# Performance work log

Hardware: AMD Instinct MI355X
Metric: run time of the kernel (lower is better)

The kernel has to match this reference:

```python
import jax, jax.numpy as jnp
import numpy as np

EMB = 768

def _mlp2(x, Wa, Wb):
    # relu(LL2(relu(LL1(x)))), bias-free linears stored as [out, in]
    return jax.nn.relu(jax.nn.relu(x @ Wa.T) @ Wb.T)

def setup_inputs() -> dict:
    key = jax.random.key(0)
    ks = jax.random.split(key, 6)
    n, m = 16, 4096  # maxlen = 64 paragraphs -> 64*64 pair slots
    X_data = jax.random.normal(ks[0], (n, 1 + m, 3 * EMB), dtype=jnp.float32)
    # first token carries num_clusters metadata (unused by the differentiable path)
    W1 = jax.random.normal(ks[1], (256, EMB), dtype=jnp.float32) * 0.02
    W2 = jax.random.normal(ks[2], (128, 256), dtype=jnp.float32) * 0.02
    W3 = jax.random.normal(ks[3], (256, EMB), dtype=jnp.float32) * 0.02
    W4 = jax.random.normal(ks[4], (128, 256), dtype=jnp.float32) * 0.02
    W5 = jax.random.normal(ks[5], (1, 128), dtype=jnp.float32) * 0.02
    return {"X_data": X_data, "W1": W1, "W2": W2, "W3": W3, "W4": W4, "W5": W5}

def reference(X_data, W1, W2, W3, W4, W5):
    # CATSCluster differentiable path: QueryScaler on X_data[:, 1:, :]
    X = X_data[:, 1:, :]                      # [n, m, 3*EMB]
    Xq = X[..., :EMB]
    Xp1 = X[..., EMB:2 * EMB]
    Xp2 = X[..., 2 * EMB:]
    Xp1z = _mlp2(Xp1, W1, W2)                 # [n, m, 128]
    Xp2z = _mlp2(Xp2, W1, W2)
    Xqz = _mlp2(Xq, W3, W4)
    Xpqz = Xqz * jnp.abs(Xp1z - Xp2z)         # [n, m, 128]
    dist = jnp.tanh(jax.nn.relu(Xpqz @ W5.T))[..., 0]  # [n, m]
    n, m = dist.shape
    p = int(np.sqrt(m))                       # maxlen
    # batch_pairscore_matrix fed to the host-side clustering step
    return dist.reshape(n, p, p)
```

## Files before the change

### kernel.cpp

```cpp
#include <hip/hip_runtime.h>
#include <hip/hip_bf16.h>


typedef short short8 __attribute__((ext_vector_type(8)));
typedef float f32x4 __attribute__((ext_vector_type(4)));

#define W1H_OFF 0u
#define W1L_OFF 196608u
#define W3H_OFF 393216u
#define W3L_OFF 589824u
#define W2H_OFF 786432u
#define W2L_OFF 819200u
#define W4H_OFF 851968u
#define W4L_OFF 884736u

__device__ __forceinline__ unsigned short bf16_rne(float f) {
  unsigned int u = __float_as_uint(f);
  u += 0x7FFFu + ((u >> 16) & 1u);
  return (unsigned short)(u >> 16);
}

__device__ __forceinline__ void split_bf16(float f, unsigned short& h, unsigned short& l) {
  h = bf16_rne(f);
  float fh = __uint_as_float(((unsigned int)h) << 16);
  l = bf16_rne(f - fh);
}

__global__ __launch_bounds__(256) void prep_weights(
    const float* __restrict__ W1, const float* __restrict__ W2,
    const float* __restrict__ W3, const float* __restrict__ W4,
    unsigned short* __restrict__ ws)
{
  int i = blockIdx.x * 256 + threadIdx.x;
  if (i < 196608) {
    unsigned short h, l;
    split_bf16(W1[i], h, l); ws[W1H_OFF + i] = h; ws[W1L_OFF + i] = l;
    split_bf16(W3[i], h, l); ws[W3H_OFF + i] = h; ws[W3L_OFF + i] = l;
    if (i < 32768) {
      split_bf16(W2[i], h, l); ws[W2H_OFF + i] = h; ws[W2L_OFF + i] = l;
      split_bf16(W4[i], h, l); ws[W4H_OFF + i] = h; ws[W4L_OFF + i] = l;
    }
  }
}

#define STRIDE_A 40
#define STRIDE_H 264

__global__ __launch_bounds__(256) void catsc_main(
    const float* __restrict__ X, const unsigned short* __restrict__ ws,
    const float* __restrict__ W5, float* __restrict__ out)
{
  __shared__ short lsA[2][2][64 * STRIDE_A];
  __shared__ short lsH[64 * STRIDE_H];
  __shared__ float lsPart[4][64];

  const int tid  = threadIdx.x;
  const int wave = tid >> 6;
  const int lane = tid & 63;
  const int l15  = lane & 15;
  const int q    = lane >> 4;
  const int blk  = blockIdx.x;

  const float* Xb = X + (size_t)((blk >> 6) * 4097 + 1 + ((blk & 63) << 6)) * 2304;

  const int srow = tid >> 3;
  const int f4   = (tid & 7) << 2;

  f32x4 z[3][4][2];

#pragma unroll
  for (int s = 0; s < 3; ++s) {
    const unsigned short* B1h = ws + (s == 0 ? W3H_OFF : W1H_OFF);
    const unsigned short* B1l = ws + (s == 0 ? W3L_OFF : W1L_OFF);
    const unsigned short* B2h = ws + (s == 0 ? W4H_OFF : W2H_OFF);
    const unsigned short* B2l = ws + (s == 0 ? W4L_OFF : W2L_OFF);
    const int so = s * 768;

    f32x4 acc[4][4];
#pragma unroll
    for (int m = 0; m < 4; ++m)
#pragma unroll
      for (int n = 0; n < 4; ++n)
        acc[m][n] = f32x4{0.f, 0.f, 0.f, 0.f};

#pragma unroll
    for (int it = 0; it < 2; ++it) {
      int rr = srow + 32 * it;
      float4 v = *(const float4*)(Xb + (size_t)rr * 2304 + so + f4);
      unsigned short h0,h1,h2,h3,l0,l1,l2,l3;
      split_bf16(v.x,h0,l0); split_bf16(v.y,h1,l1);
      split_bf16(v.z,h2,l2); split_bf16(v.w,h3,l3);
      uint2 ph, pl;
      ph.x = (unsigned)h0 | ((unsigned)h1 << 16); ph.y = (unsigned)h2 | ((unsigned)h3 << 16);
      pl.x = (unsigned)l0 | ((unsigned)l1 << 16); pl.y = (unsigned)l2 | ((unsigned)l3 << 16);
      *(uint2*)&lsA[0][0][rr * STRIDE_A + f4] = ph;
      *(uint2*)&lsA[0][1][rr * STRIDE_A + f4] = pl;
    }
    __syncthreads();

    for (int c = 0; c < 24; ++c) {
      const int b = c & 1;
      if (c + 1 < 24) {
        const int nb = b ^ 1;
#pragma unroll
        for (int it = 0; it < 2; ++it) {
          int rr = srow + 32 * it;
          float4 v = *(const float4*)(Xb + (size_t)rr * 2304 + so + (c + 1) * 32 + f4);
          unsigned short h0,h1,h2,h3,l0,l1,l2,l3;
          split_bf16(v.x,h0,l0); split_bf16(v.y,h1,l1);
          split_bf16(v.z,h2,l2); split_bf16(v.w,h3,l3);
          uint2 ph, pl;
          ph.x = (unsigned)h0 | ((unsigned)h1 << 16); ph.y = (unsigned)h2 | ((unsigned)h3 << 16);
          pl.x = (unsigned)l0 | ((unsigned)l1 << 16); pl.y = (unsigned)l2 | ((unsigned)l3 << 16);
          *(uint2*)&lsA[nb][0][rr * STRIDE_A + f4] = ph;
          *(uint2*)&lsA[nb][1][rr * STRIDE_A + f4] = pl;
        }
      }
      short8 Bh[4], Bl[4];
#pragma unroll
      for (int n = 0; n < 4; ++n) {
        size_t off = (size_t)((wave * 4 + n) * 16 + l15) * 768 + c * 32 + q * 8;
        Bh[n] = *(const short8*)(B1h + off);
        Bl[n] = *(const short8*)(B1l + off);
      }
      short8 Ah[4], Al[4];
#pragma unroll
      for (int m = 0; m < 4; ++m) {
        int a = (m * 16 + l15) * STRIDE_A + q * 8;
        Ah[m] = *(const short8*)&lsA[b][0][a];
        Al[m] = *(const short8*)&lsA[b][1][a];
      }
#pragma unroll
      for (int m = 0; m < 4; ++m)
#pragma unroll
        for (int n = 0; n < 4; ++n)
          acc[m][n] = __builtin_amdgcn_mfma_f32_16x16x32_bf16(Ah[m], Bh[n], acc[m][n], 0, 0, 0);
#pragma unroll
      for (int m = 0; m < 4; ++m)
#pragma unroll
        for (int n = 0; n < 4; ++n)
          acc[m][n] = __builtin_amdgcn_mfma_f32_16x16x32_bf16(Ah[m], Bl[n], acc[m][n], 0, 0, 0);
#pragma unroll
      for (int m = 0; m < 4; ++m)
#pragma unroll
        for (int n = 0; n < 4; ++n)
          acc[m][n] = __builtin_amdgcn_mfma_f32_16x16x32_bf16(Al[m], Bh[n], acc[m][n], 0, 0, 0);
      __syncthreads();
    }

#pragma unroll
    for (int m = 0; m < 4; ++m)
#pragma unroll
      for (int n = 0; n < 4; ++n) {
        int col = (wave * 4 + n) * 16 + l15;
#pragma unroll
        for (int i = 0; i < 4; ++i) {
          int row = m * 16 + q * 4 + i;
          lsH[row * STRIDE_H + col] = bf16_rne(fmaxf(acc[m][n][i], 0.f));
        }
      }
    __syncthreads();

    f32x4 acc2[4][2];
#pragma unroll
    for (int m = 0; m < 4; ++m)
#pragma unroll
      for (int n = 0; n < 2; ++n)
        acc2[m][n] = f32x4{0.f, 0.f, 0.f, 0.f};

    for (int c2 = 0; c2 < 8; ++c2) {
      short8 Ch[2], Cl[2];
#pragma unroll
      for (int n2 = 0; n2 < 2; ++n2) {
        size_t off = (size_t)((wave * 2 + n2) * 16 + l15) * 256 + c2 * 32 + q * 8;
        Ch[n2] = *(const short8*)(B2h + off);
        Cl[n2] = *(const short8*)(B2l + off);
      }
      short8 Ha[4];
#pragma unroll
      for (int m = 0; m < 4; ++m)
        Ha[m] = *(const short8*)&lsH[(m * 16 + l15) * STRIDE_H + c2 * 32 + q * 8];
#pragma unroll
      for (int m = 0; m < 4; ++m)
#pragma unroll
        for (int n2 = 0; n2 < 2; ++n2)
          acc2[m][n2] = __builtin_amdgcn_mfma_f32_16x16x32_bf16(Ha[m], Ch[n2], acc2[m][n2], 0, 0, 0);
#pragma unroll
      for (int m = 0; m < 4; ++m)
#pragma unroll
        for (int n2 = 0; n2 < 2; ++n2)
          acc2[m][n2] = __builtin_amdgcn_mfma_f32_16x16x32_bf16(Ha[m], Cl[n2], acc2[m][n2], 0, 0, 0);
    }
#pragma unroll
    for (int m = 0; m < 4; ++m)
#pragma unroll
      for (int n2 = 0; n2 < 2; ++n2)
#pragma unroll
        for (int i = 0; i < 4; ++i)
          z[s][m][n2][i] = fmaxf(acc2[m][n2][i], 0.f);
  }

  const float w5c0 = W5[(wave * 2 + 0) * 16 + l15];
  const float w5c1 = W5[(wave * 2 + 1) * 16 + l15];
#pragma unroll
  for (int m = 0; m < 4; ++m) {
#pragma unroll
    for (int i = 0; i < 4; ++i) {
      float v = z[0][m][0][i] * fabsf(z[1][m][0][i] - z[2][m][0][i]) * w5c0
              + z[0][m][1][i] * fabsf(z[1][m][1][i] - z[2][m][1][i]) * w5c1;
      v += __shfl_xor(v, 1);
      v += __shfl_xor(v, 2);
      v += __shfl_xor(v, 4);
      v += __shfl_xor(v, 8);
      if (l15 == 0) lsPart[wave][m * 16 + q * 4 + i] = v;
    }
  }
  __syncthreads();
  if (tid < 64) {
    float sum = lsPart[0][tid] + lsPart[1][tid] + lsPart[2][tid] + lsPart[3][tid];
    out[(size_t)blk * 64 + tid] = tanhf(fmaxf(sum, 0.f));
  }
}

extern "C" void kernel_launch(void* const* d_in, const int* in_sizes, int n_in,
                              void* d_out, int out_size, void* d_ws, size_t ws_size,
                              hipStream_t stream) {
  const float* X  = (const float*)d_in[0];
  const float* W1 = (const float*)d_in[1];
  const float* W2 = (const float*)d_in[2];
  const float* W3 = (const float*)d_in[3];
  const float* W4 = (const float*)d_in[4];
  const float* W5 = (const float*)d_in[5];
  float* out = (float*)d_out;
  unsigned short* ws = (unsigned short*)d_ws;

  prep_weights<<<dim3(768), dim3(256), 0, stream>>>(W1, W2, W3, W4, ws);
  catsc_main<<<dim3(1024), dim3(256), 0, stream>>>(X, ws, W5, out);
}
```

Baseline: 1.210 ms.

## Give each wave its own 16 rows and read X directly into MFMA fragments

The work split changes so each wave owns 16 rows across all 256 hidden columns instead of 64 rows by 64 columns. X is loaded straight from global memory into registers as A fragments, which removes the shared-memory staging, the double buffering and every block-level barrier. The per-wave hidden tile goes to a private LDS region, and the stage order is reordered so only one running z accumulator is kept, which cuts register pressure. The cost is that every wave now reads the full weight matrices from global or L2, roughly four times more weight traffic per block, and the X loads are strided per lane, so coalescing gets worse.

```diff
diff --git a/kernel.cpp b/kernel.cpp
--- a/kernel.cpp
+++ b/kernel.cpp
@@ -43,16 +43,23 @@
   }
 }
 
-#define STRIDE_A 40
+__device__ __forceinline__ void split8(const float4 a, const float4 b, short8& h, short8& l) {
+  float f[8] = {a.x, a.y, a.z, a.w, b.x, b.y, b.z, b.w};
+#pragma unroll
+  for (int j = 0; j < 8; ++j) {
+    unsigned short hh, ll;
+    split_bf16(f[j], hh, ll);
+    h[j] = (short)hh; l[j] = (short)ll;
+  }
+}
+
 #define STRIDE_H 264
 
 __global__ __launch_bounds__(256) void catsc_main(
     const float* __restrict__ X, const unsigned short* __restrict__ ws,
     const float* __restrict__ W5, float* __restrict__ out)
 {
-  __shared__ short lsA[2][2][64 * STRIDE_A];
-  __shared__ short lsH[64 * STRIDE_H];
-  __shared__ float lsPart[4][64];
+  __shared__ short lsH[4][16 * STRIDE_H];
 
   const int tid  = threadIdx.x;
   const int wave = tid >> 6;
@@ -61,164 +68,110 @@
   const int q    = lane >> 4;
   const int blk  = blockIdx.x;
 
-  const float* Xb = X + (size_t)((blk >> 6) * 4097 + 1 + ((blk & 63) << 6)) * 2304;
+  const int row = (blk >> 6) * 4097 + 1 + ((blk & 63) << 6) + wave * 16 + l15;
+  const float* Xrow = X + (size_t)row * 2304 + q * 8;
 
-  const int srow = tid >> 3;
-  const int f4   = (tid & 7) << 2;
+  short* myH = &lsH[wave][0];
 
-  f32x4 z[3][4][2];
+  f32x4 z1[8];
 
 #pragma unroll
   for (int s = 0; s < 3; ++s) {
-    const unsigned short* B1h = ws + (s == 0 ? W3H_OFF : W1H_OFF);
-    const unsigned short* B1l = ws + (s == 0 ? W3L_OFF : W1L_OFF);
-    const unsigned short* B2h = ws + (s == 0 ? W4H_OFF : W2H_OFF);
-    const unsigned short* B2l = ws + (s == 0 ? W4L_OFF : W2L_OFF);
-    const int so = s * 768;
+    const int so = (s == 0) ? 768 : (s == 1 ? 1536 : 0);
+    const unsigned short* B1h = ws + (s == 2 ? W3H_OFF : W1H_OFF);
+    const unsigned short* B1l = ws + (s == 2 ? W3L_OFF : W1L_OFF);
+    const unsigned short* B2h = ws + (s == 2 ? W4H_OFF : W2H_OFF);
+    const unsigned short* B2l = ws + (s == 2 ? W4L_OFF : W2L_OFF);
 
-    f32x4 acc[4][4];
+    f32x4 acc[16];
 #pragma unroll
-    for (int m = 0; m < 4; ++m)
-#pragma unroll
-      for (int n = 0; n < 4; ++n)
-        acc[m][n] = f32x4{0.f, 0.f, 0.f, 0.f};
+    for (int n = 0; n < 16; ++n) acc[n] = f32x4{0.f, 0.f, 0.f, 0.f};
+
+    for (int c = 0; c < 24; ++c) {
+      const float* ap = Xrow + so + c * 32;
+      float4 va = *(const float4*)(ap);
+      float4 vb = *(const float4*)(ap + 4);
+      short8 Ah, Al;
+      split8(va, vb, Ah, Al);
 
 #pragma unroll
-    for (int it = 0; it < 2; ++it) {
-      int rr = srow + 32 * it;
-      float4 v = *(const float4*)(Xb + (size_t)rr * 2304 + so + f4);
-      unsigned short h0,h1,h2,h3,l0,l1,l2,l3;
-      split_bf16(v.x,h0,l0); split_bf16(v.y,h1,l1);
-      split_bf16(v.z,h2,l2); split_bf16(v.w,h3,l3);
-      uint2 ph, pl;
-      ph.x = (unsigned)h0 | ((unsigned)h1 << 16); ph.y = (unsigned)h2 | ((unsigned)h3 << 16);
-      pl.x = (unsigned)l0 | ((unsigned)l1 << 16); pl.y = (unsigned)l2 | ((unsigned)l3 << 16);
-      *(uint2*)&lsA[0][0][rr * STRIDE_A + f4] = ph;
-      *(uint2*)&lsA[0][1][rr * STRIDE_A + f4] = pl;
-    }
-    __syncthreads();
-
-    for (int c = 0; c < 24; ++c) {
-      const int b = c & 1;
-      if (c + 1 < 24) {
-        const int nb = b ^ 1;
+      for (int half = 0; half < 2; ++half) {
+        short8 Bh[8], Bl[8];
 #pragma unroll
-        for (int it = 0; it < 2; ++it) {
-          int rr = srow + 32 * it;
-          float4 v = *(const float4*)(Xb + (size_t)rr * 2304 + so + (c + 1) * 32 + f4);
-          unsigned short h0,h1,h2,h3,l0,l1,l2,l3;
-          split_bf16(v.x,h0,l0); split_bf16(v.y,h1,l1);
-          split_bf16(v.z,h2,l2); split_bf16(v.w,h3,l3);
-          uint2 ph, pl;
-          ph.x = (unsigned)h0 | ((unsigned)h1 << 16); ph.y = (unsigned)h2 | ((unsigned)h3 << 16);
-          pl.x = (unsigned)l0 | ((unsigned)l1 << 16); pl.y = (unsigned)l2 | ((unsigned)l3 << 16);
-          *(uint2*)&lsA[nb][0][rr * STRIDE_A + f4] = ph;
-          *(uint2*)&lsA[nb][1][rr * STRIDE_A + f4] = pl;
+        for (int n = 0; n < 8; ++n) {
+          size_t off = (size_t)(((half * 8 + n) * 16 + l15) * 768 + c * 32 + q * 8);
+          Bh[n] = *(const short8*)(B1h + off);
+          Bl[n] = *(const short8*)(B1l + off);
         }
+#pragma unroll
+        for (int n = 0; n < 8; ++n)
+          acc[half * 8 + n] = __builtin_amdgcn_mfma_f32_16x16x32_bf16(Ah, Bh[n], acc[half * 8 + n], 0, 0, 0);
+#pragma unroll
+        for (int n = 0; n < 8; ++n)
+          acc[half * 8 + n] = __builtin_amdgcn_mfma_f32_16x16x32_bf16(Ah, Bl[n], acc[half * 8 + n], 0, 0, 0);
+#pragma unroll
+        for (int n = 0; n < 8; ++n)
+          acc[half * 8 + n] = __builtin_amdgcn_mfma_f32_16x16x32_bf16(Al, Bh[n], acc[half * 8 + n], 0, 0, 0);
       }
-      short8 Bh[4], Bl[4];
-#pragma unroll
-      for (int n = 0; n < 4; ++n) {
-        size_t off = (size_t)((wave * 4 + n) * 16 + l15) * 768 + c * 32 + q * 8;
-        Bh[n] = *(const short8*)(B1h + off);
-        Bl[n] = *(const short8*)(B1l + off);
-      }
-      short8 Ah[4], Al[4];
-#pragma unroll
-      for (int m = 0; m < 4; ++m) {
-        int a = (m * 16 + l15) * STRIDE_A + q * 8;
-        Ah[m] = *(const short8*)&lsA[b][0][a];
-        Al[m] = *(const short8*)&lsA[b][1][a];
-      }
-#pragma unroll
-      for (int m = 0; m < 4; ++m)
-#pragma unroll
-        for (int n = 0; n < 4; ++n)
-          acc[m][n] = __builtin_amdgcn_mfma_f32_16x16x32_bf16(Ah[m], Bh[n], acc[m][n], 0, 0, 0);
-#pragma unroll
-      for (int m = 0; m < 4; ++m)
-#pragma unroll
-        for (int n = 0; n < 4; ++n)
-          acc[m][n] = __builtin_amdgcn_mfma_f32_16x16x32_bf16(Ah[m], Bl[n], acc[m][n], 0, 0, 0);
-#pragma unroll
-      for (int m = 0; m < 4; ++m)
-#pragma unroll
-        for (int n = 0; n < 4; ++n)
-          acc[m][n] = __builtin_amdgcn_mfma_f32_16x16x32_bf16(Al[m], Bh[n], acc[m][n], 0, 0, 0);
-      __syncthreads();
     }
 
 #pragma unroll
-    for (int m = 0; m < 4; ++m)
+    for (int n = 0; n < 16; ++n)
 #pragma unroll
-      for (int n = 0; n < 4; ++n) {
-        int col = (wave * 4 + n) * 16 + l15;
+      for (int i = 0; i < 4; ++i)
+        myH[(q * 4 + i) * STRIDE_H + n * 16 + l15] = (short)bf16_rne(fmaxf(acc[n][i], 0.f));
+
+    f32x4 acc2[8];
 #pragma unroll
-        for (int i = 0; i < 4; ++i) {
-          int row = m * 16 + q * 4 + i;
-          lsH[row * STRIDE_H + col] = bf16_rne(fmaxf(acc[m][n][i], 0.f));
-        }
-      }
-    __syncthreads();
-
-    f32x4 acc2[4][2];
-#pragma unroll
-    for (int m = 0; m < 4; ++m)
-#pragma unroll
-      for (int n = 0; n < 2; ++n)
-        acc2[m][n] = f32x4{0.f, 0.f, 0.f, 0.f};
+    for (int n = 0; n < 8; ++n) acc2[n] = f32x4{0.f, 0.f, 0.f, 0.f};
 
     for (int c2 = 0; c2 < 8; ++c2) {
-      short8 Ch[2], Cl[2];
+      short8 Ha = *(const short8*)&myH[l15 * STRIDE_H + c2 * 32 + q * 8];
+      short8 Ch[8], Cl[8];
 #pragma unroll
-      for (int n2 = 0; n2 < 2; ++n2) {
-        size_t off = (size_t)((wave * 2 + n2) * 16 + l15) * 256 + c2 * 32 + q * 8;
+      for (int n2 = 0; n2 < 8; ++n2) {
+        size_t off = (size_t)((n2 * 16 + l15) * 256 + c2 * 32 + q * 8);
         Ch[n2] = *(const short8*)(B2h + off);
         Cl[n2] = *(const short8*)(B2l + off);
       }
-      short8 Ha[4];
 #pragma unroll
-      for (int m = 0; m < 4; ++m)
-        Ha[m] = *(const short8*)&lsH[(m * 16 + l15) * STRIDE_H + c2 * 32 + q * 8];
+      for (int n2 = 0; n2 < 8; ++n2)
+        acc2[n2] = __builtin_amdgcn_mfma_f32_16x16x32_bf16(Ha, Ch[n2], acc2[n2], 0, 0, 0);
 #pragma unroll
-      for (int m = 0; m < 4; ++m)
+      for (int n2 = 0; n2 < 8; ++n2)
+        acc2[n2] = __builtin_amdgcn_mfma_f32_16x16x32_bf16(Ha, Cl[n2], acc2[n2], 0, 0, 0);
+    }
+
+    if (s == 0) {
 #pragma unroll
-        for (int n2 = 0; n2 < 2; ++n2)
-          acc2[m][n2] = __builtin_amdgcn_mfma_f32_16x16x32_bf16(Ha[m], Ch[n2], acc2[m][n2], 0, 0, 0);
-#pragma unroll
-      for (int m = 0; m < 4; ++m)
-#pragma unroll
-        for (int n2 = 0; n2 < 2; ++n2)
-          acc2[m][n2] = __builtin_amdgcn_mfma_f32_16x16x32_bf16(Ha[m], Cl[n2], acc2[m][n2], 0, 0, 0);
-    }
-#pragma unroll
-    for (int m = 0; m < 4; ++m)
-#pragma unroll
-      for (int n2 = 0; n2 < 2; ++n2)
+      for (int n2 = 0; n2 < 8; ++n2)
 #pragma unroll
         for (int i = 0; i < 4; ++i)
-          z[s][m][n2][i] = fmaxf(acc2[m][n2][i], 0.f);
-  }
-
-  const float w5c0 = W5[(wave * 2 + 0) * 16 + l15];
-  const float w5c1 = W5[(wave * 2 + 1) * 16 + l15];
+          z1[n2][i] = fmaxf(acc2[n2][i], 0.f);
+    } else if (s == 1) {
 #pragma unroll
-  for (int m = 0; m < 4; ++m) {
+      for (int n2 = 0; n2 < 8; ++n2)
 #pragma unroll
-    for (int i = 0; i < 4; ++i) {
-      float v = z[0][m][0][i] * fabsf(z[1][m][0][i] - z[2][m][0][i]) * w5c0
-              + z[0][m][1][i] * fabsf(z[1][m][1][i] - z[2][m][1][i]) * w5c1;
-      v += __shfl_xor(v, 1);
-      v += __shfl_xor(v, 2);
-      v += __shfl_xor(v, 4);
-      v += __shfl_xor(v, 8);
-      if (l15 == 0) lsPart[wave][m * 16 + q * 4 + i] = v;
+        for (int i = 0; i < 4; ++i)
+          z1[n2][i] = fabsf(z1[n2][i] - fmaxf(acc2[n2][i], 0.f));
+    } else {
+      float w5c[8];
+#pragma unroll
+      for (int n2 = 0; n2 < 8; ++n2) w5c[n2] = W5[n2 * 16 + l15];
+#pragma unroll
+      for (int i = 0; i < 4; ++i) {
+        float v = 0.f;
+#pragma unroll
+        for (int n2 = 0; n2 < 8; ++n2)
+          v += fmaxf(acc2[n2][i], 0.f) * z1[n2][i] * w5c[n2];
+        v += __shfl_xor(v, 1);
+        v += __shfl_xor(v, 2);
+        v += __shfl_xor(v, 4);
+        v += __shfl_xor(v, 8);
+        if (l15 == 0)
+          out[(size_t)blk * 64 + wave * 16 + q * 4 + i] = tanhf(fmaxf(v, 0.f));
+      }
     }
-  }
-  __syncthreads();
-  if (tid < 64) {
-    float sum = lsPart[0][tid] + lsPart[1][tid] + lsPart[2][tid] + lsPart[3][tid];
-    out[(size_t)blk * 64 + tid] = tanhf(fmaxf(sum, 0.f));
   }
 }
 
```

New measurement: 1.970 ms. 1.63x slower.
